# Kernel tuning notes

Hardware: AMD Instinct MI355X
Metric: run time of the kernel (lower is better)

## Reference

```python
import jax, jax.numpy as jnp
import numpy as np

N_HEAD = 12

def setup_inputs() -> dict:
    key = jax.random.key(0)
    k1, k2, k3 = jax.random.split(key, 3)
    nx = 768
    B, S = 2, 2048
    return {
        "hidden_states": jax.random.normal(k1, (B, S, nx), dtype=jnp.float32),
        "w_attn": jax.random.normal(k2, (nx, 3 * nx), dtype=jnp.float32) * 0.02,
        "b_attn": jnp.zeros((3 * nx,), dtype=jnp.float32),
        "w_proj": jax.random.normal(k3, (nx, nx), dtype=jnp.float32) * 0.02,
        "b_proj": jnp.zeros((nx,), dtype=jnp.float32),
    }

def reference(hidden_states, w_attn, b_attn, w_proj, b_proj):
    B, S, nx = hidden_states.shape
    d_head = nx // N_HEAD
    qkv = hidden_states @ w_attn + b_attn  # [B,S,3nx]
    q, k, v = jnp.split(qkv, 3, axis=-1)
    # split heads -> [B,H,S,d]
    def split(x):
        return x.reshape(B, S, N_HEAD, d_head).transpose(0, 2, 1, 3)
    q, k, v = split(q), split(k), split(v)
    # scale=True: divide by sqrt(d_head) (v.size(-1))
    w = jnp.einsum("bhsd,bhtd->bhst", q, k) / jnp.sqrt(jnp.float32(d_head))
    w = jax.nn.softmax(w, axis=-1)
    a = jnp.einsum("bhst,bhtd->bhsd", w, v)  # [B,H,S,d]
    a = a.transpose(0, 2, 1, 3).reshape(B, S, nx)  # merge heads
    return a @ w_proj + b_proj
```

## Files before the change

kernel.cpp:

```cpp
#include <hip/hip_runtime.h>

#define NHEAD 12
#define DHEAD 64
#define SEQ   2048
#define NB    2
#define NX    768
#define MTOK  (NB * SEQ)

typedef __attribute__((ext_vector_type(8))) short short8;
typedef __attribute__((ext_vector_type(4))) short short4v;
typedef __attribute__((ext_vector_type(4))) float f32x4;

__device__ __forceinline__ unsigned short f2bf(float x) {
    union { float f; unsigned u; } v; v.f = x;
    unsigned r = v.u + 0x7fffu + ((v.u >> 16) & 1u);
    return (unsigned short)(r >> 16);
}

__device__ __forceinline__ float fexp2(float x) {
#if __has_builtin(__builtin_amdgcn_exp2f)
    return __builtin_amdgcn_exp2f(x);
#else
    float r; asm("v_exp_f32 %0, %1" : "=v"(r) : "v"(x)); return r;
#endif
}

#define MFMA32(a, b, c) __builtin_amdgcn_mfma_f32_16x16x32_bf16(a, b, c, 0, 0, 0)

__global__ __launch_bounds__(256)
void cvt_all(const float* __restrict__ hs,
             const float* __restrict__ wa, const float* __restrict__ wp,
             unsigned short* __restrict__ Abf,
             unsigned short* __restrict__ WtA, unsigned short* __restrict__ WtP)
{
    __shared__ float tile[32][33];
    const int bid = blockIdx.x;
    const int t = threadIdx.x;

    if (bid < 3072) {
        int i = bid * 256 + t;
        if (i >= 786432) return;
        float4 v = ((const float4*)hs)[i];
        ushort4 o;
        o.x = f2bf(v.x); o.y = f2bf(v.y); o.z = f2bf(v.z); o.w = f2bf(v.w);
        ((ushort4*)Abf)[i] = o;
        return;
    }

    const float* W; unsigned short* T; int K, N, bx, by;
    if (bid < 4800) {
        int b2 = bid - 3072;
        bx = b2 % 72; by = b2 / 72;
        W = wa; T = WtA; K = NX; N = 3 * NX;
    } else {
        int b2 = bid - 4800;
        bx = b2 % 24; by = b2 / 24;
        W = wp; T = WtP; K = NX; N = NX;
    }
    const int r = t >> 5, c = t & 31;
    const int k0 = by * 32, n0 = bx * 32;
#pragma unroll
    for (int i = 0; i < 4; i++)
        tile[r + i * 8][c] = W[(size_t)(k0 + r + i * 8) * N + n0 + c];
    __syncthreads();
#pragma unroll
    for (int i = 0; i < 4; i++) {
        int n = r + i * 8;
        T[(size_t)(n0 + n) * K + k0 + c] = f2bf(tile[c][n]);
    }
}

template<int MODE>
__global__ __launch_bounds__(256, 3)
void gemm_bf(const unsigned short* __restrict__ A,
             const unsigned short* __restrict__ Bt,
             const float* __restrict__ bias,
             float* __restrict__ fo,
             unsigned short* __restrict__ qb, unsigned short* __restrict__ kb2,
             unsigned short* __restrict__ vtb,
             int M, int N, int K)
{
    __shared__ __align__(16) unsigned char sm[2][16384];
    const int t = threadIdx.x;
    const int w = t >> 6, lane = t & 63;
    const int lo16 = lane & 15, quad = lane >> 4;

    const int nwg  = gridDim.x * gridDim.y;
    const int flat = blockIdx.y * gridDim.x + blockIdx.x;
    const int swz  = (flat & 7) * (nwg >> 3) + (flat >> 3);
    const int ib = (swz / gridDim.x) * 128, jb = (swz % gridDim.x) * 128;

    f32x4 acc[4][4];
#pragma unroll
    for (int mt = 0; mt < 4; mt++)
#pragma unroll
        for (int nt = 0; nt < 4; nt++) acc[mt][nt] = (f32x4){0.f, 0.f, 0.f, 0.f};

    const int srow = lane >> 2;
    const int sj   = lane & 3;

    auto stage = [&](int buf, int k0) {
#pragma unroll
        for (int i = 0; i < 4; i++) {
            const int u   = i * 4 + w;
            const int p   = u >> 3;
            const int row = (u & 7) * 16 + srow;
            const int sc  = sj ^ (row & 3);
            const unsigned short* g = (p == 0)
                ? (A  + (size_t)(ib + row) * K + k0 + sc * 8)
                : (Bt + (size_t)(jb + row) * K + k0 + sc * 8);
            void* lp = &sm[buf][p * 8192 + (u & 7) * 1024];
            __builtin_amdgcn_global_load_lds(
                (const __attribute__((address_space(1))) unsigned int*)g,
                (__attribute__((address_space(3))) unsigned int*)lp, 16, 0, 0);
        }
    };

    const int mrow = (w >> 1) * 64;
    const int nrow = (w & 1) * 64;

    stage(0, 0);
    const int NIT = K / 32;
    for (int kt = 0; kt < NIT; kt++) {
        const int buf = kt & 1;
        __syncthreads();
        if (kt + 1 < NIT) stage(buf ^ 1, (kt + 1) * 32);

        short8 af[4], bf[4];
#pragma unroll
        for (int mt = 0; mt < 4; mt++) {
            const int row = mrow + mt * 16 + lo16;
            af[mt] = *(const short8*)&sm[buf][row * 64 + ((quad ^ (row & 3)) * 16)];
        }
#pragma unroll
        for (int nt = 0; nt < 4; nt++) {
            const int row = nrow + nt * 16 + lo16;
            bf[nt] = *(const short8*)&sm[buf][8192 + row * 64 + ((quad ^ (row & 3)) * 16)];
        }
#pragma unroll
        for (int mt = 0; mt < 4; mt++)
#pragma unroll
            for (int nt = 0; nt < 4; nt++)
                acc[mt][nt] = MFMA32(af[mt], bf[nt], acc[mt][nt]);
    }

    if constexpr (MODE == 0) {
        const int which = jb / NX;
#pragma unroll
        for (int nt = 0; nt < 4; nt++) {
            const int j  = jb + nrow + nt * 16 + lo16;
            const int cc = j - which * NX;
            const int hh = cc >> 6, dd = cc & 63;
            const float bj = bias[j];
#pragma unroll
            for (int mt = 0; mt < 4; mt++) {
                const int m0 = ib + mrow + mt * 16 + quad * 4;
                const int bb = m0 >> 11;
                const int s0 = m0 & 2047;
                const size_t hb = (size_t)(bb * NHEAD + hh);
                if (which == 2) {
                    ushort4 pv;
                    pv.x = f2bf(acc[mt][nt][0] + bj);
                    pv.y = f2bf(acc[mt][nt][1] + bj);
                    pv.z = f2bf(acc[mt][nt][2] + bj);
                    pv.w = f2bf(acc[mt][nt][3] + bj);
                    *(ushort4*)(vtb + (hb * DHEAD + dd) * SEQ + s0) = pv;
                } else {
                    unsigned short* dst = (which == 0) ? qb : kb2;
                    const float sc = (which == 0) ? 0.18033688011112042f : 1.0f;
#pragma unroll
                    for (int r = 0; r < 4; r++)
                        dst[(hb * SEQ + s0 + r) * DHEAD + dd] =
                            f2bf((acc[mt][nt][r] + bj) * sc);
                }
            }
        }
    } else {
#pragma unroll
        for (int nt = 0; nt < 4; nt++) {
            const int j  = jb + nrow + nt * 16 + lo16;
            const float bj = bias[j];
#pragma unroll
            for (int mt = 0; mt < 4; mt++) {
                const int m0 = ib + mrow + mt * 16 + quad * 4;
#pragma unroll
                for (int r = 0; r < 4; r++)
                    fo[(size_t)(m0 + r) * N + j] = acc[mt][nt][r] + bj;
            }
        }
    }
}

__global__ __launch_bounds__(256, 3)
void attn_bf(const unsigned short* __restrict__ qb, const unsigned short* __restrict__ kb,
             const unsigned short* __restrict__ vtb, unsigned short* __restrict__ ab)
{
    __shared__ __align__(16) unsigned char sm[2][16384];
    const int t = threadIdx.x;
    const int w = t >> 6, lane = t & 63;
    const int lo16 = lane & 15, quad = lane >> 4;

    const int id = blockIdx.x;
    const int xcd = id & 7, slot = id >> 3;
    const int bh = xcd * 3 + slot % 3;
    const int q0 = (slot / 3) * 64;
    const int b = bh / NHEAD, h = bh % NHEAD;

    const unsigned short* Qb = qb  + (size_t)bh * SEQ * DHEAD;
    const unsigned short* Kb = kb  + (size_t)bh * SEQ * DHEAD;
    const unsigned short* Vb = vtb + (size_t)bh * DHEAD * SEQ;

    short8 qf[2];
    {
        const size_t qo = (size_t)(q0 + w * 16 + lo16) * DHEAD + quad * 8;
        qf[0] = *(const short8*)(Qb + qo);
        qf[1] = *(const short8*)(Qb + qo + 32);
    }

    const int srow = lane >> 3;
    const int sj   = lane & 7;
    auto stage = [&](int buf, int k0) {
#pragma unroll
        for (int i = 0; i < 4; i++) {
            const int u   = i * 4 + w;
            const int p   = u >> 3;
            const int row = (u & 7) * 8 + srow;
            const int sc  = sj ^ (row & 7);
            const int gr  = (row & 32) | (((row >> 2) & 3) << 3)
                          | (((row >> 4) & 1) << 2) | (row & 3);
            const unsigned short* g = (p == 0)
                ? (Kb + (size_t)(k0 + gr) * DHEAD + sc * 8)
                : (Vb + (size_t)row * SEQ + k0 + sc * 8);
            void* lp = &sm[buf][p * 8192 + (u & 7) * 1024];
            __builtin_amdgcn_global_load_lds(
                (const __attribute__((address_space(1))) unsigned int*)g,
                (__attribute__((address_space(3))) unsigned int*)lp, 16, 0, 0);
        }
    };

    f32x4 oacc[4];
#pragma unroll
    for (int dt = 0; dt < 4; dt++) oacc[dt] = (f32x4){0.f, 0.f, 0.f, 0.f};
    float lsum = 0.f;

    stage(0, 0);
    for (int kt = 0; kt < SEQ / 64; kt++) {
        const int buf = kt & 1;
        __syncthreads();
        if (kt + 1 < SEQ / 64) stage(buf ^ 1, (kt + 1) * 64);

        f32x4 s[4];
#pragma unroll
        for (int rt = 0; rt < 4; rt++) {
            const int row = rt * 16 + lo16;
            const int rs = row & 7;
            short8 kf0 = *(const short8*)&sm[buf][row * 128 + ((quad ^ rs) * 16)];
            short8 kf1 = *(const short8*)&sm[buf][row * 128 + (((4 + quad) ^ rs) * 16)];
            f32x4 a = (f32x4){0.f, 0.f, 0.f, 0.f};
            a = MFMA32(kf0, qf[0], a);
            a = MFMA32(kf1, qf[1], a);
            s[rt] = a;
        }

        short8 pf[2];
#pragma unroll
        for (int f = 0; f < 2; f++) {
            short8 pv;
#pragma unroll
            for (int r = 0; r < 4; r++) {
                float p0 = fexp2(s[2 * f][r]);
                float p1 = fexp2(s[2 * f + 1][r]);
                lsum += p0 + p1;
                pv[r]     = (short)f2bf(p0);
                pv[4 + r] = (short)f2bf(p1);
            }
            pf[f] = pv;
        }

        __builtin_amdgcn_s_setprio(1);
#pragma unroll
        for (int dt = 0; dt < 4; dt++) {
            const int row = dt * 16 + lo16;
            const int rs = row & 7;
            short8 vf0 = *(const short8*)&sm[buf][8192 + row * 128 + ((quad ^ rs) * 16)];
            short8 vf1 = *(const short8*)&sm[buf][8192 + row * 128 + (((4 + quad) ^ rs) * 16)];
            f32x4 a = oacc[dt];
            a = MFMA32(vf0, pf[0], a);
            a = MFMA32(vf1, pf[1], a);
            oacc[dt] = a;
        }
        __builtin_amdgcn_s_setprio(0);
    }

    lsum += __shfl_xor(lsum, 16);
    lsum += __shfl_xor(lsum, 32);
    const float inv = 1.0f / lsum;

    unsigned short* dst = ab + (size_t)(b * SEQ + q0 + w * 16 + lo16) * NX + h * DHEAD;
#pragma unroll
    for (int dt = 0; dt < 4; dt++) {
        ushort4 pv;
        pv.x = f2bf(oacc[dt][0] * inv);
        pv.y = f2bf(oacc[dt][1] * inv);
        pv.z = f2bf(oacc[dt][2] * inv);
        pv.w = f2bf(oacc[dt][3] * inv);
        *(ushort4*)(dst + dt * 16 + quad * 4) = pv;
    }
}

extern "C" void kernel_launch(void* const* d_in, const int* in_sizes, int n_in,
                              void* d_out, int out_size, void* d_ws, size_t ws_size,
                              hipStream_t stream)
{
    const float* hs     = (const float*)d_in[0];
    const float* w_attn = (const float*)d_in[1];
    const float* b_attn = (const float*)d_in[2];
    const float* w_proj = (const float*)d_in[3];
    const float* b_proj = (const float*)d_in[4];
    float* out = (float*)d_out;

    unsigned short* wsu = (unsigned short*)d_ws;
    unsigned short* Abf  = wsu;
    unsigned short* WtA  = Abf  + 3145728;
    unsigned short* WtP  = WtA  + 1769472;
    unsigned short* qbuf = WtP  + 589824;
    unsigned short* kbuf = qbuf + 3145728;
    unsigned short* vtbf = kbuf + 3145728;
    unsigned short* abf  = vtbf + 3145728;

    cvt_all<<<5376, 256, 0, stream>>>(hs, w_attn, w_proj, Abf, WtA, WtP);

    gemm_bf<0><<<dim3(18, 32), 256, 0, stream>>>(
        Abf, WtA, b_attn, nullptr, qbuf, kbuf, vtbf, MTOK, 3 * NX, NX);

    attn_bf<<<768, 256, 0, stream>>>(qbuf, kbuf, vtbf, abf);

    gemm_bf<1><<<dim3(6, 32), 256, 0, stream>>>(
        abf, WtP, b_proj, out, nullptr, nullptr, nullptr, MTOK, NX, NX);
}
```

Baseline: 151.9 us.

## Stage V-transpose stores through LDS and use packed bf16 convert in softmax

For the V part of the QKV projection, the epilogue now writes bias-added bf16 results into a swizzled shared-memory tile. It then reads them back as 16-byte rows, so the transposed V tensor gets wide coalesced global stores instead of scattered 8-byte writes. This adds two barriers and reuses the GEMM shared buffer. In the attention loop, the per-element software bf16 rounding is replaced with the hardware v_cvt_pk_bf16_f32 packed convert, and the row-sum adds are rebalanced into a tree. That cuts ALU work on the exp-to-P path, though rounding may differ slightly.

Measured after the change: 153.7 us. No clear change (+1.1%).

```diff
diff --git a/kernel.cpp b/kernel.cpp
--- a/kernel.cpp
+++ b/kernel.cpp
@@ -15,6 +15,12 @@
     union { float f; unsigned u; } v; v.f = x;
     unsigned r = v.u + 0x7fffu + ((v.u >> 16) & 1u);
     return (unsigned short)(r >> 16);
+}
+
+__device__ __forceinline__ unsigned pkbf(float a, float b) {
+    unsigned r;
+    asm("v_cvt_pk_bf16_f32 %0, %1, %2" : "=v"(r) : "v"(a), "v"(b));
+    return r;
 }
 
 __device__ __forceinline__ float fexp2(float x) {
@@ -146,26 +152,52 @@
 
     if constexpr (MODE == 0) {
         const int which = jb / NX;
-#pragma unroll
-        for (int nt = 0; nt < 4; nt++) {
-            const int j  = jb + nrow + nt * 16 + lo16;
-            const int cc = j - which * NX;
-            const int hh = cc >> 6, dd = cc & 63;
-            const float bj = bias[j];
-#pragma unroll
-            for (int mt = 0; mt < 4; mt++) {
-                const int m0 = ib + mrow + mt * 16 + quad * 4;
-                const int bb = m0 >> 11;
-                const int s0 = m0 & 2047;
-                const size_t hb = (size_t)(bb * NHEAD + hh);
-                if (which == 2) {
+        if (which == 2) {
+            __syncthreads();
+            char* smT = (char*)sm;
+#pragma unroll
+            for (int nt = 0; nt < 4; nt++) {
+                const int jl = nrow + nt * 16 + lo16;
+                const float bj = bias[jb + jl];
+#pragma unroll
+                for (int mt = 0; mt < 4; mt++) {
+                    const int dw0 = (mrow >> 1) + mt * 8 + quad * 2;
+                    const int dws = dw0 ^ ((jl & 15) << 2);
                     ushort4 pv;
                     pv.x = f2bf(acc[mt][nt][0] + bj);
                     pv.y = f2bf(acc[mt][nt][1] + bj);
                     pv.z = f2bf(acc[mt][nt][2] + bj);
                     pv.w = f2bf(acc[mt][nt][3] + bj);
-                    *(ushort4*)(vtb + (hb * DHEAD + dd) * SEQ + s0) = pv;
-                } else {
+                    *(ushort4*)(smT + jl * 256 + dws * 4) = pv;
+                }
+            }
+            __syncthreads();
+            const int bb2 = ib >> 11, sbase = ib & 2047;
+#pragma unroll
+            for (int i = 0; i < 8; i++) {
+                const int idx = i * 256 + t;
+                const int jr  = idx >> 4;
+                const int c8  = idx & 15;
+                const int pc  = c8 ^ (jr & 15);
+                short8 vv = *(const short8*)(smT + jr * 256 + pc * 16);
+                const int cc2 = jb - 2 * NX + jr;
+                const int hh2 = cc2 >> 6, dd2 = cc2 & 63;
+                *(short8*)(vtb + ((size_t)(bb2 * NHEAD + hh2) * DHEAD + dd2) * SEQ
+                           + sbase + c8 * 8) = vv;
+            }
+        } else {
+#pragma unroll
+            for (int nt = 0; nt < 4; nt++) {
+                const int j  = jb + nrow + nt * 16 + lo16;
+                const int cc = j - which * NX;
+                const int hh = cc >> 6, dd = cc & 63;
+                const float bj = bias[j];
+#pragma unroll
+                for (int mt = 0; mt < 4; mt++) {
+                    const int m0 = ib + mrow + mt * 16 + quad * 4;
+                    const int bb = m0 >> 11;
+                    const int s0 = m0 & 2047;
+                    const size_t hb = (size_t)(bb * NHEAD + hh);
                     unsigned short* dst = (which == 0) ? qb : kb2;
                     const float sc = (which == 0) ? 0.18033688011112042f : 1.0f;
 #pragma unroll
@@ -265,16 +297,17 @@
         short8 pf[2];
 #pragma unroll
         for (int f = 0; f < 2; f++) {
-            short8 pv;
-#pragma unroll
-            for (int r = 0; r < 4; r++) {
-                float p0 = fexp2(s[2 * f][r]);
-                float p1 = fexp2(s[2 * f + 1][r]);
-                lsum += p0 + p1;
-                pv[r]     = (short)f2bf(p0);
-                pv[4 + r] = (short)f2bf(p1);
-            }
-            pf[f] = pv;
+            float e0 = fexp2(s[2 * f][0]),     e1 = fexp2(s[2 * f][1]);
+            float e2 = fexp2(s[2 * f][2]),     e3 = fexp2(s[2 * f][3]);
+            float e4 = fexp2(s[2 * f + 1][0]), e5 = fexp2(s[2 * f + 1][1]);
+            float e6 = fexp2(s[2 * f + 1][2]), e7 = fexp2(s[2 * f + 1][3]);
+            lsum += ((e0 + e1) + (e2 + e3)) + ((e4 + e5) + (e6 + e7));
+            union { short8 s8; unsigned u[4]; } pk;
+            pk.u[0] = pkbf(e0, e1);
+            pk.u[1] = pkbf(e2, e3);
+            pk.u[2] = pkbf(e4, e5);
+            pk.u[3] = pkbf(e6, e7);
+            pf[f] = pk.s8;
         }
 
         __builtin_amdgcn_s_setprio(1);
```
